# Kernel tuning notes

Hardware: AMD Instinct MI355X
Metric: run time of the kernel (lower is better)

## Reference

```python
import jax, jax.numpy as jnp
import numpy as np

NU, NI, E, NNZ, NLAYERS, TOPK = 2560, 3584, 64, 200000, 2, 5
N = NU + NI
DQK = 4 * E  # Linear(dim, 4*dim)


def setup_inputs() -> dict:
    key = jax.random.key(0)
    ks = jax.random.split(key, 14)
    s = 1.0 / np.sqrt(E)
    return {
        "user_emb": jax.random.normal(ks[0], (NU, E), jnp.float32) * s,
        "item_emb": jax.random.normal(ks[1], (NI, E), jnp.float32) * s,
        "norm_rows": jax.random.randint(ks[2], (NNZ,), 0, N, jnp.int32),
        "norm_cols": jax.random.randint(ks[3], (NNZ,), 0, N, jnp.int32),
        "norm_vals": jax.random.uniform(ks[4], (NNZ,), jnp.float32) / 32.0,
        "adj_rows": jax.random.randint(ks[5], (NNZ,), 0, N, jnp.int32),
        "adj_cols": jax.random.randint(ks[6], (NNZ,), 0, N, jnp.int32),
        "adj_vals": jnp.ones((NNZ,), jnp.float32),
        "Wq": jax.random.normal(ks[7], (DQK, E), jnp.float32) * s,
        "bq": jnp.zeros((DQK,), jnp.float32),
        "Wk": jax.random.normal(ks[8], (DQK, E), jnp.float32) * s,
        "bk": jnp.zeros((DQK,), jnp.float32),
        "Wv": jax.random.normal(ks[9], (DQK, E), jnp.float32) * s,
        "bv": jnp.zeros((DQK,), jnp.float32),
    }


def reference(user_emb, item_emb, norm_rows, norm_cols, norm_vals,
              adj_rows, adj_cols, adj_vals, Wq, bq, Wk, bk, Wv, bv):
    # densified sparse adjacencies (duplicates accumulated, as COO spmm would)
    A_norm = jnp.zeros((N, N), jnp.float32).at[norm_rows, norm_cols].add(norm_vals)
    A = jnp.zeros((N, N), jnp.float32).at[adj_rows, adj_cols].add(adj_vals)

    ego = jnp.concatenate([user_emb, item_emb], axis=0)  # [N, E]
    layers = []
    att_out = None
    for _ in range(NLAYERS):
        layers.append(ego)
        # GNN propagation: sparse.mm(norm_adj, ego)
        ego = A_norm @ ego  # [N, E]
        # dense similarity + sparse-blended similarity
        sim = ego @ ego.T                      # [N, N]
        sim = sim + 0.5 * (A @ sim)            # [N, N]
        # top-K neighbor selection + gather
        _, idx = jax.lax.top_k(sim, TOPK)      # [N, K]
        sample = ego[idx]                      # [N, K, E]
        # SampleAttention: Linear(dim, 4*dim) Q/K/V, scaled dot-product over K neighbors
        q = ego @ Wq.T + bq                    # [N, 4E]
        kk = sample @ Wk.T + bk                # [N, K, 4E]
        vv = sample @ Wv.T + bv                # [N, K, 4E]
        scores = jnp.einsum('nd,nkd->nk', q, kk) / jnp.sqrt(jnp.float32(DQK))
        att = jax.nn.softmax(scores, axis=-1)
        att_out = jnp.einsum('nk,nkd->nd', att, vv)  # [N, 4E]
    mean_emb = jnp.mean(jnp.stack(layers, axis=1), axis=1)  # [N, E]
    return mean_emb[:NU], mean_emb[NU:], att_out
```

## Files before the change

### kernel.cpp

```cpp
#include <hip/hip_runtime.h>
#include <math.h>

#define NUSER 2560
#define NITEM 3584
#define NN    6144
#define EDIM  64
#define NNZ   200000
#define DQK   256
#define KTOP  5
#define SPLITS 8
#define TPS    6
#define CK     8
#define ELLW   96
#define TPB   256
#define NBUILD 1563
#define BSTR  72

typedef __attribute__((ext_vector_type(8))) short bf16x8;
typedef __attribute__((ext_vector_type(4))) float f32x4;

__device__ __forceinline__ unsigned short f2bf(float f) {
    unsigned int b = __float_as_uint(f);
    unsigned int r = (b + 0x7FFFu + ((b >> 16) & 1u)) >> 16;
    return (unsigned short)r;
}
__device__ __forceinline__ int pack2(float a, float b) {
    return (int)f2bf(a) | ((int)f2bf(b) << 16);
}
__device__ __forceinline__ void ell_unpack(long long v, int* col, float* w) {
    *col = (int)(v & 0xffffffffLL);
    *w   = __int_as_float((int)(v >> 32));
}

__global__ void build_kernel(const int* __restrict__ nr, const int* __restrict__ nc,
                             const float* __restrict__ nv,
                             const int* __restrict__ ar, const int* __restrict__ ac,
                             const float* __restrict__ Wq, const float* __restrict__ Wk,
                             const float* __restrict__ bq,
                             int* __restrict__ cnt_n, int* __restrict__ cnt_a,
                             long long* __restrict__ cv_n, int* __restrict__ cv_a,
                             float* __restrict__ Gbuf) {
    __shared__ float gq[4096];
    __shared__ float gk[4096];
    int t = threadIdx.x;

    if (blockIdx.x == NBUILD) {
        float accG[16];
#pragma unroll
        for (int i = 0; i < 16; ++i) accG[i] = 0.f;
        float uacc = 0.f;
        int e = t >> 2, fb = (t & 3) * 16;
        for (int d0 = 0; d0 < DQK; d0 += 64) {
            __syncthreads();
#pragma unroll
            for (int i = 0; i < 16; ++i) {
                int v = i * 256 + t;
                gq[v] = Wq[d0 * 64 + v];
                gk[v] = Wk[d0 * 64 + v];
            }
            __syncthreads();
            for (int dc = 0; dc < 64; ++dc) {
                float a = gq[dc * 64 + e];
                float4 w0 = *(const float4*)&gk[dc * 64 + fb];
                float4 w1 = *(const float4*)&gk[dc * 64 + fb + 4];
                float4 w2 = *(const float4*)&gk[dc * 64 + fb + 8];
                float4 w3 = *(const float4*)&gk[dc * 64 + fb + 12];
                accG[0]  = fmaf(a, w0.x, accG[0]);  accG[1]  = fmaf(a, w0.y, accG[1]);
                accG[2]  = fmaf(a, w0.z, accG[2]);  accG[3]  = fmaf(a, w0.w, accG[3]);
                accG[4]  = fmaf(a, w1.x, accG[4]);  accG[5]  = fmaf(a, w1.y, accG[5]);
                accG[6]  = fmaf(a, w1.z, accG[6]);  accG[7]  = fmaf(a, w1.w, accG[7]);
                accG[8]  = fmaf(a, w2.x, accG[8]);  accG[9]  = fmaf(a, w2.y, accG[9]);
                accG[10] = fmaf(a, w2.z, accG[10]); accG[11] = fmaf(a, w2.w, accG[11]);
                accG[12] = fmaf(a, w3.x, accG[12]); accG[13] = fmaf(a, w3.y, accG[13]);
                accG[14] = fmaf(a, w3.z, accG[14]); accG[15] = fmaf(a, w3.w, accG[15]);
            }
            if (t < 64) {
                for (int dc = 0; dc < 64; ++dc)
                    uacc = fmaf(bq[d0 + dc], gk[dc * 64 + t], uacc);
            }
        }
#pragma unroll
        for (int i = 0; i < 16; ++i) Gbuf[e * 64 + fb + i] = accG[i];
        if (t < 64) Gbuf[4096 + t] = uacc;
        return;
    }

    int g = blockIdx.x * TPB + t;
    if (g < NNZ) {
        int r = nr[g], c = nc[g];
        float v = nv[g];
        int slot = atomicAdd(&cnt_n[r], 1);
        long long pk = (unsigned int)c | ((long long)(unsigned int)__float_as_int(v) << 32);
        cv_n[r * ELLW + slot] = pk;
    } else if (g < 2 * NNZ) {
        int h = g - NNZ;
        int r = ar[h], c = ac[h];
        int slot = atomicAdd(&cnt_a[r], 1);
        cv_a[r * ELLW + slot] = c;
    }
}

__global__ __launch_bounds__(TPB) void spmm_ell_emb_kernel(
        const int* __restrict__ cnt, const long long* __restrict__ cv,
        const float* __restrict__ user, const float* __restrict__ item,
        float* __restrict__ dst) {
    int r = blockIdx.x * 4 + (threadIdx.x >> 6);
    int lane = threadIdx.x & 63;
    int s = r * ELLW, e = s + cnt[r];
    float a[8];
#pragma unroll
    for (int u = 0; u < 8; ++u) a[u] = 0.f;
    int j = s, n8 = s + ((e - s) & ~7);
    for (; j < n8; j += 8) {
        int col[8]; float w[8];
#pragma unroll
        for (int u = 0; u < 8; ++u) ell_unpack(cv[j + u], &col[u], &w[u]);
#pragma unroll
        for (int u = 0; u < 8; ++u) {
            float x = (col[u] < NUSER) ? user[col[u] * EDIM + lane]
                                       : item[(col[u] - NUSER) * EDIM + lane];
            a[u] = fmaf(w[u], x, a[u]);
        }
    }
    for (; j < e; ++j) {
        int col; float w;
        ell_unpack(cv[j], &col, &w);
        float x = (col < NUSER) ? user[col * EDIM + lane] : item[(col - NUSER) * EDIM + lane];
        a[0] = fmaf(w, x, a[0]);
    }
    dst[r * EDIM + lane] = ((a[0] + a[1]) + (a[2] + a[3])) + ((a[4] + a[5]) + (a[6] + a[7]));
}

__global__ __launch_bounds__(TPB) void spmm_ell_kernel(
        const int* __restrict__ cnt, const long long* __restrict__ cv,
        const float* __restrict__ src, float* __restrict__ dst) {
    int r = blockIdx.x * 4 + (threadIdx.x >> 6);
    int lane = threadIdx.x & 63;
    int s = r * ELLW, e = s + cnt[r];
    float a[8];
#pragma unroll
    for (int u = 0; u < 8; ++u) a[u] = 0.f;
    int j = s, n8 = s + ((e - s) & ~7);
    for (; j < n8; j += 8) {
        int col[8]; float w[8];
#pragma unroll
        for (int u = 0; u < 8; ++u) ell_unpack(cv[j + u], &col[u], &w[u]);
#pragma unroll
        for (int u = 0; u < 8; ++u)
            a[u] = fmaf(w[u], src[col[u] * EDIM + lane], a[u]);
    }
    for (; j < e; ++j) {
        int col; float w;
        ell_unpack(cv[j], &col, &w);
        a[0] = fmaf(w, src[col * EDIM + lane], a[0]);
    }
    dst[r * EDIM + lane] = ((a[0] + a[1]) + (a[2] + a[3])) + ((a[4] + a[5]) + (a[6] + a[7]));
}

__global__ __launch_bounds__(TPB) void qm_mean_kernel(
        const int* __restrict__ cnt, const int* __restrict__ cv,
        const float* __restrict__ ego2, const float* __restrict__ ego1,
        const float* __restrict__ user, const float* __restrict__ item,
        const float* __restrict__ Gbuf,
        float* __restrict__ Qm, float* __restrict__ outmean, float* __restrict__ P) {
    __shared__ float Gs[4160];
    int t = threadIdx.x;

    if (blockIdx.x >= NN / 4) {
        int pb = blockIdx.x - NN / 4;
#pragma unroll
        for (int i = 0; i < 17; ++i) {
            int v = i * 256 + t;
            if (v < 4160) Gs[v] = Gbuf[v];
        }
        __syncthreads();
        int r = pb * 64 + (t >> 2), fb = (t & 3) * 16;
        const float4* row4 = (const float4*)(ego2 + (size_t)r * EDIM);
        float4 rw[16];
#pragma unroll
        for (int i = 0; i < 16; ++i) rw[i] = row4[i];
        float4 acc0 = *(const float4*)&Gs[4096 + fb];
        float4 acc1 = *(const float4*)&Gs[4096 + fb + 4];
        float4 acc2 = *(const float4*)&Gs[4096 + fb + 8];
        float4 acc3 = *(const float4*)&Gs[4096 + fb + 12];
#pragma unroll
        for (int ee = 0; ee < 16; ++ee) {
            float av[4] = {rw[ee].x, rw[ee].y, rw[ee].z, rw[ee].w};
#pragma unroll
            for (int q = 0; q < 4; ++q) {
                int e = ee * 4 + q;
                float a = av[q];
                float4 g0 = *(const float4*)&Gs[e * 64 + fb];
                float4 g1 = *(const float4*)&Gs[e * 64 + fb + 4];
                float4 g2 = *(const float4*)&Gs[e * 64 + fb + 8];
                float4 g3 = *(const float4*)&Gs[e * 64 + fb + 12];
                acc0.x = fmaf(a, g0.x, acc0.x); acc0.y = fmaf(a, g0.y, acc0.y);
                acc0.z = fmaf(a, g0.z, acc0.z); acc0.w = fmaf(a, g0.w, acc0.w);
                acc1.x = fmaf(a, g1.x, acc1.x); acc1.y = fmaf(a, g1.y, acc1.y);
                acc1.z = fmaf(a, g1.z, acc1.z); acc1.w = fmaf(a, g1.w, acc1.w);
                acc2.x = fmaf(a, g2.x, acc2.x); acc2.y = fmaf(a, g2.y, acc2.y);
                acc2.z = fmaf(a, g2.z, acc2.z); acc2.w = fmaf(a, g2.w, acc2.w);
                acc3.x = fmaf(a, g3.x, acc3.x); acc3.y = fmaf(a, g3.y, acc3.y);
                acc3.z = fmaf(a, g3.z, acc3.z); acc3.w = fmaf(a, g3.w, acc3.w);
            }
        }
        float4* dst = (float4*)(P + (size_t)r * EDIM + fb);
        dst[0] = acc0; dst[1] = acc1; dst[2] = acc2; dst[3] = acc3;
        return;
    }

    int r = blockIdx.x * 4 + (t >> 6);
    int lane = t & 63;
    int s = r * ELLW, e = s + cnt[r];
    float a[8];
#pragma unroll
    for (int u = 0; u < 8; ++u) a[u] = 0.f;
    int j = s, n8 = s + ((e - s) & ~7);
    for (; j < n8; j += 8) {
        int col[8];
#pragma unroll
        for (int u = 0; u < 8; ++u) col[u] = cv[j + u];
#pragma unroll
        for (int u = 0; u < 8; ++u)
            a[u] += ego2[col[u] * EDIM + lane];
    }
    for (; j < e; ++j) a[0] += ego2[cv[j] * EDIM + lane];
    float acc = ((a[0] + a[1]) + (a[2] + a[3])) + ((a[4] + a[5]) + (a[6] + a[7]));
    int o = r * EDIM + lane;
    Qm[o] = ego2[o] + 0.5f * acc;
    float e0v = (r < NUSER) ? user[o] : item[o - NUSER * EDIM];
    outmean[o] = 0.5f * (e0v + ego1[o]);
}

__device__ __forceinline__ void ins3(float v, int ci, float tv[3], int ti[3]) {
    if (v > tv[2]) {
        bool p1 = v > tv[1], p0 = v > tv[0];
        tv[2] = p1 ? tv[1] : v;  ti[2] = p1 ? ti[1] : ci;
        if (p1) { tv[1] = p0 ? tv[0] : v; ti[1] = p0 ? ti[0] : ci; }
        if (p0) { tv[0] = v; ti[0] = ci; }
    }
}

__global__ __launch_bounds__(TPB, 6) void topk_kernel(
        const float* __restrict__ ego2, const float* __restrict__ Qm,
        int* __restrict__ pidx) {
    __shared__ __align__(16) short smem[13312];
    int t = threadIdx.x;
    int rb = blockIdx.x % 96, sp = blockIdx.x / 96;
    int r0 = rb * 64;
    int w = t >> 6, lane = t & 63, lq = lane >> 4, lc = lane & 15;

    short* Ah = smem;
    short* Bh = smem + 4096;

    {
        int row = t >> 2, seg = t & 3;
        const float4* src = (const float4*)&Qm[(size_t)(r0 + row) * EDIM + seg * 16];
        float4 f0 = src[0], f1 = src[1], f2 = src[2], f3 = src[3];
        int4 p0, p1;
        p0.x = pack2(f0.x, f0.y); p0.y = pack2(f0.z, f0.w);
        p0.z = pack2(f1.x, f1.y); p0.w = pack2(f1.z, f1.w);
        p1.x = pack2(f2.x, f2.y); p1.y = pack2(f2.z, f2.w);
        p1.z = pack2(f3.x, f3.y); p1.w = pack2(f3.z, f3.w);
        *(int4*)&Ah[row * EDIM + seg * 16] = p0;
        *(int4*)&Ah[row * EDIM + seg * 16 + 8] = p1;
    }

    float4 pa[4], pb[4];
    {
        int c0 = (sp * TPS) * 128;
#pragma unroll
        for (int rep = 0; rep < 4; ++rep) {
            int v = t + 256 * rep;
            const float4* src = (const float4*)&ego2[(size_t)(c0 + (v >> 3)) * EDIM + (v & 7) * 8];
            pa[rep] = src[0]; pb[rep] = src[1];
        }
    }

    float t3v[4][3]; int t3i[4][3];
#pragma unroll
    for (int i = 0; i < 4; ++i)
#pragma unroll
        for (int k = 0; k < 3; ++k) { t3v[i][k] = -INFINITY; t3i[i][k] = 0x7fffffff; }

    bf16x8 af0, af1;
    for (int tile = 0; tile < TPS; ++tile) {
        int c0 = (sp * TPS + tile) * 128;
        __syncthreads();
        {
#pragma unroll
            for (int rep = 0; rep < 4; ++rep) {
                int v = t + 256 * rep;
                int4 q;
                q.x = pack2(pa[rep].x, pa[rep].y); q.y = pack2(pa[rep].z, pa[rep].w);
                q.z = pack2(pb[rep].x, pb[rep].y); q.w = pack2(pb[rep].z, pb[rep].w);
                *(int4*)&Bh[(v >> 3) * BSTR + (v & 7) * 8] = q;
            }
        }
        if (tile + 1 < TPS) {
            int c1 = c0 + 128;
#pragma unroll
            for (int rep = 0; rep < 4; ++rep) {
                int v = t + 256 * rep;
                const float4* src = (const float4*)&ego2[(size_t)(c1 + (v >> 3)) * EDIM + (v & 7) * 8];
                pa[rep] = src[0]; pb[rep] = src[1];
            }
        }
        __syncthreads();
        if (tile == 0) {
            af0 = *(const bf16x8*)&Ah[(w * 16 + lc) * EDIM + lq * 8];
            af1 = *(const bf16x8*)&Ah[(w * 16 + lc) * EDIM + 32 + lq * 8];
        }

#pragma unroll
        for (int ch = 0; ch < 8; ++ch) {
            bf16x8 b0 = *(const bf16x8*)&Bh[(ch * 16 + lc) * BSTR + lq * 8];
            bf16x8 b1 = *(const bf16x8*)&Bh[(ch * 16 + lc) * BSTR + 32 + lq * 8];
            f32x4 acc = {0.f, 0.f, 0.f, 0.f};
            acc = __builtin_amdgcn_mfma_f32_16x16x32_bf16(af0, b0, acc, 0, 0, 0);
            acc = __builtin_amdgcn_mfma_f32_16x16x32_bf16(af1, b1, acc, 0, 0, 0);
            int ci = c0 + ch * 16 + lc;
#pragma unroll
            for (int reg = 0; reg < 4; ++reg)
                ins3(acc[reg], ci, t3v[reg], t3i[reg]);
        }
    }

#pragma unroll
    for (int i = 0; i < 4; ++i) {
        int row = r0 + w * 16 + lq * 4 + i;
        int ptr = 0;
        for (int k = 0; k < CK; ++k) {
            float cvv = (ptr == 0) ? t3v[i][0] : (ptr == 1) ? t3v[i][1]
                      : (ptr == 2) ? t3v[i][2] : -INFINITY;
            int   cii = (ptr == 0) ? t3i[i][0] : (ptr == 1) ? t3i[i][1]
                      : (ptr == 2) ? t3i[i][2] : 0x7fffffff;
            float bv = cvv; int bi = cii;
#pragma unroll
            for (int off = 1; off < 16; off <<= 1) {
                float ov = __shfl_xor(bv, off, 64);
                int   oi = __shfl_xor(bi, off, 64);
                if (ov > bv || (ov == bv && oi < bi)) { bv = ov; bi = oi; }
            }
            if (bv == cvv && bi == cii) ptr++;
            if (lc == 0) pidx[(row * SPLITS + sp) * CK + k] = bi;
        }
    }
}

__global__ __launch_bounds__(TPB) void attn_sel_kernel(
        const float* __restrict__ Qm, const float* __restrict__ P,
        const float* __restrict__ ego2, const int* __restrict__ pidx,
        float* __restrict__ m) {
    __shared__ float sb[4][64];
    __shared__ float sa[4][64];
    int wv = threadIdx.x >> 6, lane = threadIdx.x & 63;
    int r = blockIdx.x * 4 + wv;
    int ci0 = pidx[r * 64 + lane];
    int part = lane & 3;

    const float4* qmp = (const float4*)(Qm + (size_t)r * EDIM + part * 16);
    float4 q0 = qmp[0], q1 = qmp[1], q2 = qmp[2], q3 = qmp[3];
    const float4* pmp = (const float4*)(P + (size_t)r * EDIM + part * 16);
    float4 p0 = pmp[0], p1 = pmp[1], p2 = pmp[2], p3 = pmp[3];

#pragma unroll
    for (int p = 0; p < 4; ++p) {
        int j = p * 16 + (lane >> 2);
        int c = __shfl(ci0, j, 64);
        const float4* ep = (const float4*)(ego2 + (size_t)c * EDIM + part * 16);
        float4 e0 = ep[0], e1 = ep[1], e2 = ep[2], e3 = ep[3];
        float s = 0.f, s2 = 0.f;
        s = fmaf(q0.x, e0.x, s); s = fmaf(q0.y, e0.y, s); s = fmaf(q0.z, e0.z, s); s = fmaf(q0.w, e0.w, s);
        s = fmaf(q1.x, e1.x, s); s = fmaf(q1.y, e1.y, s); s = fmaf(q1.z, e1.z, s); s = fmaf(q1.w, e1.w, s);
        s = fmaf(q2.x, e2.x, s); s = fmaf(q2.y, e2.y, s); s = fmaf(q2.z, e2.z, s); s = fmaf(q2.w, e2.w, s);
        s = fmaf(q3.x, e3.x, s); s = fmaf(q3.y, e3.y, s); s = fmaf(q3.z, e3.z, s); s = fmaf(q3.w, e3.w, s);
        s2 = fmaf(p0.x, e0.x, s2); s2 = fmaf(p0.y, e0.y, s2); s2 = fmaf(p0.z, e0.z, s2); s2 = fmaf(p0.w, e0.w, s2);
        s2 = fmaf(p1.x, e1.x, s2); s2 = fmaf(p1.y, e1.y, s2); s2 = fmaf(p1.z, e1.z, s2); s2 = fmaf(p1.w, e1.w, s2);
        s2 = fmaf(p2.x, e2.x, s2); s2 = fmaf(p2.y, e2.y, s2); s2 = fmaf(p2.z, e2.z, s2); s2 = fmaf(p2.w, e2.w, s2);
        s2 = fmaf(p3.x, e3.x, s2); s2 = fmaf(p3.y, e3.y, s2); s2 = fmaf(p3.z, e3.z, s2); s2 = fmaf(p3.w, e3.w, s2);
        s  += __shfl_xor(s, 1, 64);  s  += __shfl_xor(s, 2, 64);
        s2 += __shfl_xor(s2, 1, 64); s2 += __shfl_xor(s2, 2, 64);
        if (part == 0) { sb[wv][j] = s; sa[wv][j] = s2; }
    }
    float sv = sb[wv][lane];
    float av = sa[wv][lane];

    float prevv = INFINITY; int previ = -1;
    int cI[KTOP]; float atk[KTOP];
#pragma unroll
    for (int k = 0; k < KTOP; ++k) {
        bool adm = (sv < prevv) || (sv == prevv && ci0 > previ);
        float bv = adm ? sv : -INFINITY;
        int   bi = adm ? ci0 : 0x7fffffff;
        float ba = av;
#pragma unroll
        for (int off = 1; off < 64; off <<= 1) {
            float ov = __shfl_xor(bv, off, 64);
            int   oi = __shfl_xor(bi, off, 64);
            float oa = __shfl_xor(ba, off, 64);
            if (ov > bv || (ov == bv && oi < bi)) { bv = ov; bi = oi; ba = oa; }
        }
        cI[k] = bi; atk[k] = ba; prevv = bv; previ = bi;
    }

    float sc[KTOP];
#pragma unroll
    for (int k = 0; k < KTOP; ++k) sc[k] = atk[k] * 0.0625f;
    float mx = sc[0];
#pragma unroll
    for (int k = 1; k < KTOP; ++k) mx = fmaxf(mx, sc[k]);
    float wgt[KTOP], ssum = 0.f;
#pragma unroll
    for (int k = 0; k < KTOP; ++k) { wgt[k] = expf(sc[k] - mx); ssum += wgt[k]; }
    float inv = 1.f / ssum;

    float mm = 0.f;
#pragma unroll
    for (int k = 0; k < KTOP; ++k)
        mm = fmaf(wgt[k] * inv, ego2[(size_t)cI[k] * EDIM + lane], mm);
    m[(size_t)r * EDIM + lane] = mm;
}

__global__ __launch_bounds__(TPB, 3) void gemm_kernel(
        const float* __restrict__ A, const float* __restrict__ W,
        const float* __restrict__ b, float* __restrict__ out) {
    __shared__ __align__(16) float smem[64 * 64 + 128 * 64];
    float* As = smem;
    float* Bs = smem + 4096;
    int t = threadIdx.x, tx = t & 15, ty = t >> 4;
    int r0 = blockIdx.x * 64, d0 = blockIdx.y * 128;
    {
        int r = t & 63, eb = (t >> 6) * 16;
#pragma unroll
        for (int rep = 0; rep < 4; ++rep) {
            int e0 = eb + rep * 4;
            float4 v = *(const float4*)&A[(r0 + r) * EDIM + e0];
            As[(e0 + 0) * 64 + r] = v.x; As[(e0 + 1) * 64 + r] = v.y;
            As[(e0 + 2) * 64 + r] = v.z; As[(e0 + 3) * 64 + r] = v.w;
        }
    }
    {
        int d = t & 127, eb = (t >> 7) * 32;
#pragma unroll
        for (int rep = 0; rep < 8; ++rep) {
            int e0 = eb + rep * 4;
            float4 v = *(const float4*)&W[(d0 + d) * EDIM + e0];
            Bs[(e0 + 0) * 128 + d] = v.x; Bs[(e0 + 1) * 128 + d] = v.y;
            Bs[(e0 + 2) * 128 + d] = v.z; Bs[(e0 + 3) * 128 + d] = v.w;
        }
    }
    __syncthreads();
    float acc[4][8];
#pragma unroll
    for (int i = 0; i < 4; ++i)
#pragma unroll
        for (int j = 0; j < 8; ++j) acc[i][j] = 0.f;
#pragma unroll 4
    for (int e = 0; e < 64; ++e) {
        float4 a  = *(const float4*)&As[e * 64 + ty * 4];
        float4 b0 = *(const float4*)&Bs[e * 128 + tx * 4];
        float4 b1 = *(const float4*)&Bs[e * 128 + 64 + tx * 4];
        float ar[4] = {a.x, a.y, a.z, a.w};
#pragma unroll
        for (int i = 0; i < 4; ++i) {
            acc[i][0] = fmaf(ar[i], b0.x, acc[i][0]);
            acc[i][1] = fmaf(ar[i], b0.y, acc[i][1]);
            acc[i][2] = fmaf(ar[i], b0.z, acc[i][2]);
            acc[i][3] = fmaf(ar[i], b0.w, acc[i][3]);
            acc[i][4] = fmaf(ar[i], b1.x, acc[i][4]);
            acc[i][5] = fmaf(ar[i], b1.y, acc[i][5]);
            acc[i][6] = fmaf(ar[i], b1.z, acc[i][6]);
            acc[i][7] = fmaf(ar[i], b1.w, acc[i][7]);
        }
    }
    float4 bias0 = *(const float4*)&b[d0 + tx * 4];
    float4 bias1 = *(const float4*)&b[d0 + 64 + tx * 4];
#pragma unroll
    for (int i = 0; i < 4; ++i) {
        int r = r0 + ty * 4 + i;
        float4 o0 = make_float4(acc[i][0] + bias0.x, acc[i][1] + bias0.y,
                                acc[i][2] + bias0.z, acc[i][3] + bias0.w);
        float4 o1 = make_float4(acc[i][4] + bias1.x, acc[i][5] + bias1.y,
                                acc[i][6] + bias1.z, acc[i][7] + bias1.w);
        *(float4*)&out[r * DQK + d0 + tx * 4] = o0;
        *(float4*)&out[r * DQK + d0 + 64 + tx * 4] = o1;
    }
}

extern "C" void kernel_launch(void* const* d_in, const int* in_sizes, int n_in,
                              void* d_out, int out_size, void* d_ws, size_t ws_size,
                              hipStream_t stream) {
    const float* user  = (const float*)d_in[0];
    const float* item  = (const float*)d_in[1];
    const int*   nrows = (const int*)d_in[2];
    const int*   ncols = (const int*)d_in[3];
    const float* nvals = (const float*)d_in[4];
    const int*   arows = (const int*)d_in[5];
    const int*   acols = (const int*)d_in[6];
    const float* Wq = (const float*)d_in[8];  const float* bq = (const float*)d_in[9];
    const float* Wk = (const float*)d_in[10];
    const float* Wv = (const float*)d_in[12]; const float* bv = (const float*)d_in[13];
    float* out = (float*)d_out;
    float* ws  = (float*)d_ws;

    const int NE = NN * EDIM;
    float* ego1 = ws;
    float* ego2 = ws + NE;
    float* Qm   = ws + 2 * NE;
    float* P    = ws + 3 * NE;
    float* m    = ws + 4 * NE;
    int*   pidx = (int*)(ws + 5 * NE);
    float* Gbuf = ws + 6 * NE;
    int*   ell  = (int*)(ws + 6 * NE + 4160);
    int* cnt_n  = ell;
    int* cnt_a  = ell + 6144;
    long long* cv_n = (long long*)(ell + 12288);
    int* cv_a   = (int*)(cv_n + NN * ELLW);

    hipMemsetAsync(cnt_n, 0, 12288 * sizeof(int), stream);
    build_kernel<<<NBUILD + 1, TPB, 0, stream>>>(nrows, ncols, nvals, arows, acols,
                                                 Wq, Wk, bq,
                                                 cnt_n, cnt_a, cv_n, cv_a, Gbuf);
    spmm_ell_emb_kernel<<<NN / 4, TPB, 0, stream>>>(cnt_n, cv_n, user, item, ego1);
    spmm_ell_kernel<<<NN / 4, TPB, 0, stream>>>(cnt_n, cv_n, ego1, ego2);
    qm_mean_kernel<<<NN / 4 + 96, TPB, 0, stream>>>(cnt_a, cv_a, ego2, ego1, user, item,
                                                    Gbuf, Qm, out, P);
    topk_kernel<<<96 * SPLITS, TPB, 0, stream>>>(ego2, Qm, pidx);
    attn_sel_kernel<<<NN / 4, TPB, 0, stream>>>(Qm, P, ego2, pidx, m);
    gemm_kernel<<<dim3(NN / 64, DQK / 128), TPB, 0, stream>>>(m, Wv, bv, out + NE);
}
```

Measured before the change: 230.2 us.

## Fuse Wv projection into attention kernel and double top-k split count

The separate GEMM that applied Wv and bias to the attention-weighted neighbor mix is removed. Each wavefront now computes its row's 256-wide output directly from the 64-element mixed vector, with weights read from global/L1. The top-k kernel is also split into 16 partitions of 3 tiles instead of 8 of 6, so the attention kernel merges 128 candidates per row. This removes one launch and the intermediate m buffer round-trip, and raises parallelism in top-k. The cost is per-row uncached-style Wv reads (64 KB per row, served from cache) and a larger candidate merge.

```diff
diff --git a/kernel.cpp b/kernel.cpp
--- a/kernel.cpp
+++ b/kernel.cpp
@@ -8,8 +8,8 @@
 #define NNZ   200000
 #define DQK   256
 #define KTOP  5
-#define SPLITS 8
-#define TPS    6
+#define SPLITS 16
+#define TPS    3
 #define CK     8
 #define ELLW   96
 #define TPB   256
@@ -351,12 +351,14 @@
 __global__ __launch_bounds__(TPB) void attn_sel_kernel(
         const float* __restrict__ Qm, const float* __restrict__ P,
         const float* __restrict__ ego2, const int* __restrict__ pidx,
-        float* __restrict__ m) {
-    __shared__ float sb[4][64];
-    __shared__ float sa[4][64];
+        const float* __restrict__ Wv, const float* __restrict__ bv_,
+        float* __restrict__ out) {
+    __shared__ float sb[4][128];
+    __shared__ float sa[4][128];
     int wv = threadIdx.x >> 6, lane = threadIdx.x & 63;
     int r = blockIdx.x * 4 + wv;
-    int ci0 = pidx[r * 64 + lane];
+    int ci0 = pidx[r * 128 + lane];
+    int ci1 = pidx[r * 128 + 64 + lane];
     int part = lane & 3;
 
     const float4* qmp = (const float4*)(Qm + (size_t)r * EDIM + part * 16);
@@ -365,9 +367,9 @@
     float4 p0 = pmp[0], p1 = pmp[1], p2 = pmp[2], p3 = pmp[3];
 
 #pragma unroll
-    for (int p = 0; p < 4; ++p) {
+    for (int p = 0; p < 8; ++p) {
         int j = p * 16 + (lane >> 2);
-        int c = __shfl(ci0, j, 64);
+        int c = (j < 64) ? __shfl(ci0, j, 64) : __shfl(ci1, j - 64, 64);
         const float4* ep = (const float4*)(ego2 + (size_t)c * EDIM + part * 16);
         float4 e0 = ep[0], e1 = ep[1], e2 = ep[2], e3 = ep[3];
         float s = 0.f, s2 = 0.f;
@@ -383,17 +385,19 @@
         s2 += __shfl_xor(s2, 1, 64); s2 += __shfl_xor(s2, 2, 64);
         if (part == 0) { sb[wv][j] = s; sa[wv][j] = s2; }
     }
-    float sv = sb[wv][lane];
-    float av = sa[wv][lane];
+    float sv0 = sb[wv][lane],      av0 = sa[wv][lane];
+    float sv1 = sb[wv][64 + lane], av1 = sa[wv][64 + lane];
 
     float prevv = INFINITY; int previ = -1;
     int cI[KTOP]; float atk[KTOP];
 #pragma unroll
     for (int k = 0; k < KTOP; ++k) {
-        bool adm = (sv < prevv) || (sv == prevv && ci0 > previ);
-        float bv = adm ? sv : -INFINITY;
-        int   bi = adm ? ci0 : 0x7fffffff;
-        float ba = av;
+        bool adm0 = (sv0 < prevv) || (sv0 == prevv && ci0 > previ);
+        bool adm1 = (sv1 < prevv) || (sv1 == prevv && ci1 > previ);
+        float bv = adm0 ? sv0 : -INFINITY;
+        int   bi = adm0 ? ci0 : 0x7fffffff;
+        float ba = av0;
+        if (adm1 && (sv1 > bv || (sv1 == bv && ci1 < bi))) { bv = sv1; bi = ci1; ba = av1; }
 #pragma unroll
         for (int off = 1; off < 64; off <<= 1) {
             float ov = __shfl_xor(bv, off, 64);
@@ -419,73 +423,26 @@
 #pragma unroll
     for (int k = 0; k < KTOP; ++k)
         mm = fmaf(wgt[k] * inv, ego2[(size_t)cI[k] * EDIM + lane], mm);
-    m[(size_t)r * EDIM + lane] = mm;
-}
-
-__global__ __launch_bounds__(TPB, 3) void gemm_kernel(
-        const float* __restrict__ A, const float* __restrict__ W,
-        const float* __restrict__ b, float* __restrict__ out) {
-    __shared__ __align__(16) float smem[64 * 64 + 128 * 64];
-    float* As = smem;
-    float* Bs = smem + 4096;
-    int t = threadIdx.x, tx = t & 15, ty = t >> 4;
-    int r0 = blockIdx.x * 64, d0 = blockIdx.y * 128;
-    {
-        int r = t & 63, eb = (t >> 6) * 16;
-#pragma unroll
-        for (int rep = 0; rep < 4; ++rep) {
-            int e0 = eb + rep * 4;
-            float4 v = *(const float4*)&A[(r0 + r) * EDIM + e0];
-            As[(e0 + 0) * 64 + r] = v.x; As[(e0 + 1) * 64 + r] = v.y;
-            As[(e0 + 2) * 64 + r] = v.z; As[(e0 + 3) * 64 + r] = v.w;
-        }
-    }
-    {
-        int d = t & 127, eb = (t >> 7) * 32;
-#pragma unroll
-        for (int rep = 0; rep < 8; ++rep) {
-            int e0 = eb + rep * 4;
-            float4 v = *(const float4*)&W[(d0 + d) * EDIM + e0];
-            Bs[(e0 + 0) * 128 + d] = v.x; Bs[(e0 + 1) * 128 + d] = v.y;
-            Bs[(e0 + 2) * 128 + d] = v.z; Bs[(e0 + 3) * 128 + d] = v.w;
-        }
-    }
-    __syncthreads();
-    float acc[4][8];
-#pragma unroll
-    for (int i = 0; i < 4; ++i)
-#pragma unroll
-        for (int j = 0; j < 8; ++j) acc[i][j] = 0.f;
-#pragma unroll 4
-    for (int e = 0; e < 64; ++e) {
-        float4 a  = *(const float4*)&As[e * 64 + ty * 4];
-        float4 b0 = *(const float4*)&Bs[e * 128 + tx * 4];
-        float4 b1 = *(const float4*)&Bs[e * 128 + 64 + tx * 4];
-        float ar[4] = {a.x, a.y, a.z, a.w};
-#pragma unroll
-        for (int i = 0; i < 4; ++i) {
-            acc[i][0] = fmaf(ar[i], b0.x, acc[i][0]);
-            acc[i][1] = fmaf(ar[i], b0.y, acc[i][1]);
-            acc[i][2] = fmaf(ar[i], b0.z, acc[i][2]);
-            acc[i][3] = fmaf(ar[i], b0.w, acc[i][3]);
-            acc[i][4] = fmaf(ar[i], b1.x, acc[i][4]);
-            acc[i][5] = fmaf(ar[i], b1.y, acc[i][5]);
-            acc[i][6] = fmaf(ar[i], b1.z, acc[i][6]);
-            acc[i][7] = fmaf(ar[i], b1.w, acc[i][7]);
-        }
-    }
-    float4 bias0 = *(const float4*)&b[d0 + tx * 4];
-    float4 bias1 = *(const float4*)&b[d0 + 64 + tx * 4];
-#pragma unroll
-    for (int i = 0; i < 4; ++i) {
-        int r = r0 + ty * 4 + i;
-        float4 o0 = make_float4(acc[i][0] + bias0.x, acc[i][1] + bias0.y,
-                                acc[i][2] + bias0.z, acc[i][3] + bias0.w);
-        float4 o1 = make_float4(acc[i][4] + bias1.x, acc[i][5] + bias1.y,
-                                acc[i][6] + bias1.z, acc[i][7] + bias1.w);
-        *(float4*)&out[r * DQK + d0 + tx * 4] = o0;
-        *(float4*)&out[r * DQK + d0 + 64 + tx * 4] = o1;
-    }
+
+    int d0 = lane * 4;
+    float4 oacc = *(const float4*)&bv_[d0];
+    for (int e0 = 0; e0 < 64; e0 += 4) {
+        float m0 = __shfl(mm, e0, 64), m1 = __shfl(mm, e0 + 1, 64);
+        float m2 = __shfl(mm, e0 + 2, 64), m3 = __shfl(mm, e0 + 3, 64);
+        float4 w0 = *(const float4*)&Wv[(d0 + 0) * EDIM + e0];
+        float4 w1 = *(const float4*)&Wv[(d0 + 1) * EDIM + e0];
+        float4 w2 = *(const float4*)&Wv[(d0 + 2) * EDIM + e0];
+        float4 w3 = *(const float4*)&Wv[(d0 + 3) * EDIM + e0];
+        oacc.x = fmaf(m0, w0.x, oacc.x); oacc.x = fmaf(m1, w0.y, oacc.x);
+        oacc.x = fmaf(m2, w0.z, oacc.x); oacc.x = fmaf(m3, w0.w, oacc.x);
+        oacc.y = fmaf(m0, w1.x, oacc.y); oacc.y = fmaf(m1, w1.y, oacc.y);
+        oacc.y = fmaf(m2, w1.z, oacc.y); oacc.y = fmaf(m3, w1.w, oacc.y);
+        oacc.z = fmaf(m0, w2.x, oacc.z); oacc.z = fmaf(m1, w2.y, oacc.z);
+        oacc.z = fmaf(m2, w2.z, oacc.z); oacc.z = fmaf(m3, w2.w, oacc.z);
+        oacc.w = fmaf(m0, w3.x, oacc.w); oacc.w = fmaf(m1, w3.y, oacc.w);
+        oacc.w = fmaf(m2, w3.z, oacc.w); oacc.w = fmaf(m3, w3.w, oacc.w);
+    }
+    *(float4*)&out[(size_t)r * DQK + d0] = oacc;
 }
 
 extern "C" void kernel_launch(void* const* d_in, const int* in_sizes, int n_in,
@@ -500,7 +457,7 @@
     const int*   acols = (const int*)d_in[6];
     const float* Wq = (const float*)d_in[8];  const float* bq = (const float*)d_in[9];
     const float* Wk = (const float*)d_in[10];
-    const float* Wv = (const float*)d_in[12]; const float* bv = (const float*)d_in[13];
+    const float* Wv = (const float*)d_in[12]; const float* bvp = (const float*)d_in[13];
     float* out = (float*)d_out;
     float* ws  = (float*)d_ws;
 
@@ -509,8 +466,7 @@
     float* ego2 = ws + NE;
     float* Qm   = ws + 2 * NE;
     float* P    = ws + 3 * NE;
-    float* m    = ws + 4 * NE;
-    int*   pidx = (int*)(ws + 5 * NE);
+    int*   pidx = (int*)(ws + 4 * NE);
     float* Gbuf = ws + 6 * NE;
     int*   ell  = (int*)(ws + 6 * NE + 4160);
     int* cnt_n  = ell;
@@ -527,6 +483,5 @@
     qm_mean_kernel<<<NN / 4 + 96, TPB, 0, stream>>>(cnt_a, cv_a, ego2, ego1, user, item,
                                                     Gbuf, Qm, out, P);
     topk_kernel<<<96 * SPLITS, TPB, 0, stream>>>(ego2, Qm, pidx);
-    attn_sel_kernel<<<NN / 4, TPB, 0, stream>>>(Qm, P, ego2, pidx, m);
-    gemm_kernel<<<dim3(NN / 64, DQK / 128), TPB, 0, stream>>>(m, Wv, bv, out + NE);
-}
+    attn_sel_kernel<<<NN / 4, TPB, 0, stream>>>(Qm, P, ego2, pidx, Wv, bvp, out + NE);
+}
```

Measured after the change: 265.2 us. 1.15x slower.
